# Kernel tuning notes

Hardware: AMD Instinct MI355X
Metric: run time of the kernel (lower is better)

Reference implementation:

```python
import jax, jax.numpy as jnp
import numpy as np

NUM_HEADS = 64
NUM_KV_HEADS = 8
HEAD_DIM = 128
Q_MULT = NUM_HEADS // NUM_KV_HEADS  # 8
CACHE_LEN = 8192
SLIDING_WINDOW = 4096
BATCH = 16
SM_SCALE = 1.0 / float(np.sqrt(HEAD_DIM))


def setup_inputs() -> dict:
    key = jax.random.key(0)
    k1, k2, k3, k4, k5 = jax.random.split(key, 5)
    return {
        "Q": jax.random.normal(k1, (BATCH, 1, NUM_HEADS * HEAD_DIM), dtype=jnp.float32),
        "K": jax.random.normal(k2, (BATCH, 1, NUM_KV_HEADS * HEAD_DIM), dtype=jnp.float32),
        "V": jax.random.normal(k3, (BATCH, 1, NUM_KV_HEADS * HEAD_DIM), dtype=jnp.float32),
        "K_cache": jax.random.normal(k4, (BATCH, CACHE_LEN, NUM_KV_HEADS * HEAD_DIM), dtype=jnp.float32),
        "V_cache": jax.random.normal(k5, (BATCH, CACHE_LEN, NUM_KV_HEADS * HEAD_DIM), dtype=jnp.float32),
        "sinks": jnp.zeros((NUM_HEADS,), dtype=jnp.float32),
    }


def reference(Q, K, V, K_cache, V_cache, sinks):
    B = Q.shape[0]
    total_len = CACHE_LEN + 1
    # reshape to (B, kv_heads, q_mult, d) / (B, len, kv_heads, d)
    q = Q.reshape(B, NUM_KV_HEADS, Q_MULT, HEAD_DIM)
    k_new = K.reshape(B, 1, NUM_KV_HEADS, HEAD_DIM)
    v_new = V.reshape(B, 1, NUM_KV_HEADS, HEAD_DIM)
    k_full = jnp.concatenate([K_cache.reshape(B, CACHE_LEN, NUM_KV_HEADS, HEAD_DIM), k_new], axis=1)
    v_full = jnp.concatenate([V_cache.reshape(B, CACHE_LEN, NUM_KV_HEADS, HEAD_DIM), v_new], axis=1)

    # scores: (B, kv_heads, q_mult, total_len) -- GQA: each kv head serves q_mult query heads
    qk = jnp.einsum("bhmd,bkhd->bhmk", q, k_full) * SM_SCALE

    # sliding-window mask (static shapes: total_len > window here)
    if SLIDING_WINDOW > 0 and total_len > SLIDING_WINDOW:
        pos = jnp.arange(total_len)
        qk = jnp.where(pos[None, None, None, :] < total_len - SLIDING_WINDOW, -jnp.inf, qk)

    # append sink logit per query head, softmax, then drop sink column
    s = sinks.reshape(1, NUM_KV_HEADS, Q_MULT, 1)
    logits = jnp.concatenate([qk, jnp.broadcast_to(s, (B, NUM_KV_HEADS, Q_MULT, 1))], axis=-1)
    w = jax.nn.softmax(logits, axis=-1)[..., :-1]

    attn = jnp.einsum("bhmk,bkhd->bhmd", w, v_full)
    return attn.reshape(B, 1, NUM_HEADS * HEAD_DIM)
```

## Files before the change

kernel.cpp:

```cpp
#include <hip/hip_runtime.h>
#include <math.h>

#define BATCH 16
#define KVH 8
#define QM 8
#define NH 64
#define HD 128
#define CACHE 8192
#define WIN 4096
#define PSTART (CACHE + 1 - WIN)
#define KSTRIDE (KVH * HD)
#define REC_FLOATS (2 * QM + QM * HD)
#define SM_SCALE 0.08838834764831845f

#define BCAST(x, imm) __int_as_float(__builtin_amdgcn_ds_swizzle(__float_as_int(x), (imm)))

#define SCALE_ACC(h, rr) { acc[h].x *= rr; acc[h].y *= rr; acc[h].z *= rr; acc[h].w *= rr; }
#define PV_ACC(h, ww)    { acc[h].x += ww*vc4.x; acc[h].y += ww*vc4.y; acc[h].z += ww*vc4.z; acc[h].w += ww*vc4.w; }

template <int NSPLIT, bool EDGE>
__device__ __forceinline__ void attn_body(
    int c, int b, int t,
    const float* __restrict__ Q, const float* __restrict__ Knew,
    const float* __restrict__ Vnew, const float* __restrict__ Kc,
    const float* __restrict__ Vc, float* __restrict__ ws) {
    constexpr int SPAN = WIN / NSPLIT;
    static_assert(SPAN % 2 == 0, "unroll-2");
    const int g  = t >> 5;
    const int dp = t & 31;
    const int pb = PSTART + c * SPAN;

    float4 q4[8];
    {
        const float* qp = Q + ((size_t)b * NH + (size_t)g * QM) * HD + dp * 4;
        #pragma unroll
        for (int h = 0; h < 8; ++h) {
            float4 v = *reinterpret_cast<const float4*>(qp + h * HD);
            q4[h] = make_float4(v.x * SM_SCALE, v.y * SM_SCALE,
                                v.z * SM_SCALE, v.w * SM_SCALE);
        }
    }

    const float* kb_ = Kc + ((size_t)b * CACHE + pb) * KSTRIDE + t * 4;
    const float* vb_ = Vc + ((size_t)b * CACHE + pb) * KSTRIDE + t * 4;
    const float* kn_ = Knew + (size_t)b * KSTRIDE + t * 4;
    const float* vn_ = Vnew + (size_t)b * KSTRIDE + t * 4;

    auto LK = [&](int j) -> float4 {
        const float* a = kb_ + (size_t)j * KSTRIDE;
        if (EDGE && (pb + j >= CACHE)) a = kn_;
        return *reinterpret_cast<const float4*>(a);
    };
    auto LV = [&](int j) -> float4 {
        const float* a = vb_ + (size_t)j * KSTRIDE;
        if (EDGE && (pb + j >= CACHE)) a = vn_;
        return *reinterpret_cast<const float4*>(a);
    };

    float4 acc[8];
    #pragma unroll
    for (int h = 0; h < 8; ++h) acc[h] = make_float4(0.f, 0.f, 0.f, 0.f);
    float mrun = -INFINITY, lrun = 0.f;

    auto STEP = [&](float4 kc4, float4 vc4) {
        float p0 = q4[0].x*kc4.x + q4[0].y*kc4.y + q4[0].z*kc4.z + q4[0].w*kc4.w;
        float p1 = q4[1].x*kc4.x + q4[1].y*kc4.y + q4[1].z*kc4.z + q4[1].w*kc4.w;
        float p2 = q4[2].x*kc4.x + q4[2].y*kc4.y + q4[2].z*kc4.z + q4[2].w*kc4.w;
        float p3 = q4[3].x*kc4.x + q4[3].y*kc4.y + q4[3].z*kc4.z + q4[3].w*kc4.w;
        float p4 = q4[4].x*kc4.x + q4[4].y*kc4.y + q4[4].z*kc4.z + q4[4].w*kc4.w;
        float p5 = q4[5].x*kc4.x + q4[5].y*kc4.y + q4[5].z*kc4.z + q4[5].w*kc4.w;
        float p6 = q4[6].x*kc4.x + q4[6].y*kc4.y + q4[6].z*kc4.z + q4[6].w*kc4.w;
        float p7 = q4[7].x*kc4.x + q4[7].y*kc4.y + q4[7].z*kc4.z + q4[7].w*kc4.w;
        const bool s1 = dp & 1;
        float a0 = (s1?p1:p0) + __shfl_xor((s1?p0:p1), 1);
        float a1 = (s1?p3:p2) + __shfl_xor((s1?p2:p3), 1);
        float a2 = (s1?p5:p4) + __shfl_xor((s1?p4:p5), 1);
        float a3 = (s1?p7:p6) + __shfl_xor((s1?p6:p7), 1);
        const bool s2 = dp & 2;
        float b0 = (s2?a1:a0) + __shfl_xor((s2?a0:a1), 2);
        float b1 = (s2?a3:a2) + __shfl_xor((s2?a2:a3), 2);
        const bool s4 = dp & 4;
        float s = (s4?b1:b0) + __shfl_xor((s4?b0:b1), 4);
        s += __shfl_xor(s, 8);
        s += __shfl_xor(s, 16);

        if (__any(s > mrun + 8.0f)) {
            float mn = fmaxf(mrun, s);
            float rs = __expf(mrun - mn);
            mrun = mn; lrun *= rs;
            float r0 = BCAST(rs, 0x00); SCALE_ACC(0, r0);
            float r1 = BCAST(rs, 0x20); SCALE_ACC(1, r1);
            float r2 = BCAST(rs, 0x40); SCALE_ACC(2, r2);
            float r3 = BCAST(rs, 0x60); SCALE_ACC(3, r3);
            float r4 = BCAST(rs, 0x80); SCALE_ACC(4, r4);
            float r5 = BCAST(rs, 0xA0); SCALE_ACC(5, r5);
            float r6 = BCAST(rs, 0xC0); SCALE_ACC(6, r6);
            float r7 = BCAST(rs, 0xE0); SCALE_ACC(7, r7);
        }
        float e = __expf(s - mrun);
        lrun += e;
        float w0 = BCAST(e, 0x00); PV_ACC(0, w0);
        float w1 = BCAST(e, 0x20); PV_ACC(1, w1);
        float w2 = BCAST(e, 0x40); PV_ACC(2, w2);
        float w3 = BCAST(e, 0x60); PV_ACC(3, w3);
        float w4 = BCAST(e, 0x80); PV_ACC(4, w4);
        float w5 = BCAST(e, 0xA0); PV_ACC(5, w5);
        float w6 = BCAST(e, 0xC0); PV_ACC(6, w6);
        float w7 = BCAST(e, 0xE0); PV_ACC(7, w7);
    };

    float4 ka = LK(0), va = LV(0), kb4 = LK(1), vb4 = LV(1);
    for (int j = 0; j < SPAN; j += 2) {
        float4 k0 = ka, v0 = va;
        ka = LK(j + 2); va = LV(j + 2);
        STEP(k0, v0);
        float4 k1 = kb4, v1 = vb4;
        kb4 = LK(j + 3); vb4 = LV(j + 3);
        STEP(k1, v1);
    }

    float* rec = ws + ((size_t)(b * KVH + g) * NSPLIT + c) * REC_FLOATS;
    if (dp < 8) { rec[dp] = mrun; rec[QM + dp] = lrun; }
    #pragma unroll
    for (int h = 0; h < 8; ++h)
        *reinterpret_cast<float4*>(rec + 2 * QM + h * HD + dp * 4) = acc[h];
}

template <int NSPLIT>
__global__ __launch_bounds__(256, 4)
void attn_partial(const float* __restrict__ Q, const float* __restrict__ Knew,
                  const float* __restrict__ Vnew, const float* __restrict__ Kc,
                  const float* __restrict__ Vc, float* __restrict__ ws) {
    const int c = blockIdx.x, b = blockIdx.y, t = threadIdx.x;
    if (c == NSPLIT - 1)
        attn_body<NSPLIT, true >(c, b, t, Q, Knew, Vnew, Kc, Vc, ws);
    else
        attn_body<NSPLIT, false>(c, b, t, Q, Knew, Vnew, Kc, Vc, ws);
}

template <int NC>
__global__ __launch_bounds__(256)
void attn_combine(const float* __restrict__ ws, const float* __restrict__ sinks,
                  float* __restrict__ out) {
    const int kvh = blockIdx.x, b = blockIdx.y, t = threadIdx.x;
    const int h = t >> 5, lp = t & 31;
    const float* base = ws + (size_t)(b * KVH + kvh) * NC * REC_FLOATS;

    float M0 = -INFINITY, d0 = 0.f, M1 = -INFINITY, d1 = 0.f;
    float4 o0 = make_float4(0.f, 0.f, 0.f, 0.f);
    float4 o1 = make_float4(0.f, 0.f, 0.f, 0.f);

    #pragma unroll 2
    for (int cc = 0; cc < NC; cc += 2) {
        {
            const float* rec = base + (size_t)cc * REC_FLOATS;
            float mc = rec[h], lc = rec[QM + h];
            float4 a = *reinterpret_cast<const float4*>(rec + 2*QM + h*HD + 4*lp);
            float Mn = fmaxf(M0, mc);
            float fo = __expf(M0 - Mn), fc = __expf(mc - Mn);
            d0 = d0 * fo + fc * lc;
            o0.x = o0.x*fo + fc*a.x; o0.y = o0.y*fo + fc*a.y;
            o0.z = o0.z*fo + fc*a.z; o0.w = o0.w*fo + fc*a.w;
            M0 = Mn;
        }
        {
            const float* rec = base + (size_t)(cc + 1) * REC_FLOATS;
            float mc = rec[h], lc = rec[QM + h];
            float4 a = *reinterpret_cast<const float4*>(rec + 2*QM + h*HD + 4*lp);
            float Mn = fmaxf(M1, mc);
            float fo = __expf(M1 - Mn), fc = __expf(mc - Mn);
            d1 = d1 * fo + fc * lc;
            o1.x = o1.x*fo + fc*a.x; o1.y = o1.y*fo + fc*a.y;
            o1.z = o1.z*fo + fc*a.z; o1.w = o1.w*fo + fc*a.w;
            M1 = Mn;
        }
    }

    const float sk = sinks[kvh * QM + h];
    float M = fmaxf(fmaxf(M0, M1), sk);
    float f0 = __expf(M0 - M), f1 = __expf(M1 - M);
    float d = d0 * f0 + d1 * f1 + __expf(sk - M);
    float inv = 1.f / d;
    float4 r;
    r.x = (o0.x*f0 + o1.x*f1) * inv;
    r.y = (o0.y*f0 + o1.y*f1) * inv;
    r.z = (o0.z*f0 + o1.z*f1) * inv;
    r.w = (o0.w*f0 + o1.w*f1) * inv;
    float* op = out + (size_t)b * NH * HD + (size_t)(kvh * QM + h) * HD + 4 * lp;
    *reinterpret_cast<float4*>(op) = r;
}

template <int NSPLIT>
static void launch_nc(const float* Q, const float* K, const float* V,
                      const float* Kc, const float* Vc, const float* sinks,
                      float* out, float* ws, hipStream_t stream) {
    dim3 g1(NSPLIT, BATCH);
    attn_partial<NSPLIT><<<g1, 256, 0, stream>>>(Q, K, V, Kc, Vc, ws);
    dim3 g2(KVH, BATCH);
    attn_combine<NSPLIT><<<g2, 256, 0, stream>>>(ws, sinks, out);
}

extern "C" void kernel_launch(void* const* d_in, const int* in_sizes, int n_in,
                              void* d_out, int out_size, void* d_ws, size_t ws_size,
                              hipStream_t stream) {
    const float* Q     = (const float*)d_in[0];
    const float* K     = (const float*)d_in[1];
    const float* V     = (const float*)d_in[2];
    const float* Kc    = (const float*)d_in[3];
    const float* Vc    = (const float*)d_in[4];
    const float* sinks = (const float*)d_in[5];
    float* out = (float*)d_out;
    float* ws  = (float*)d_ws;

    auto need = [](int nc) {
        return (size_t)BATCH * KVH * nc * REC_FLOATS * sizeof(float);
    };
    if (ws_size >= need(64))      launch_nc<64>(Q, K, V, Kc, Vc, sinks, out, ws, stream);
    else if (ws_size >= need(32)) launch_nc<32>(Q, K, V, Kc, Vc, sinks, out, ws, stream);
    else                          launch_nc<16>(Q, K, V, Kc, Vc, sinks, out, ws, stream);
}
```

Measured before the change: 122.0 us.

## Parallelize split-K combine with warp-reduced weights and split head-dim grid

The combine kernel now computes the global max and denominator for each query head with warp shuffles, producing normalized per-split weights in shared memory. A serial online-softmax chain over splits is no longer needed. The head dimension is split across a new grid z-dimension of 4, and each block divides the splits among 4 thread groups, summing their partials through LDS. This adds parallelism and removes the dependent exp chain in a small tail kernel, at the cost of extra barriers and redundant weight computation per z-block. The NC=16 fallback is also dropped.

```diff
diff --git a/kernel.cpp b/kernel.cpp
--- a/kernel.cpp
+++ b/kernel.cpp
@@ -142,52 +142,62 @@
 __global__ __launch_bounds__(256)
 void attn_combine(const float* __restrict__ ws, const float* __restrict__ sinks,
                   float* __restrict__ out) {
-    const int kvh = blockIdx.x, b = blockIdx.y, t = threadIdx.x;
-    const int h = t >> 5, lp = t & 31;
+    static_assert(NC == 32 || NC == 64, "NC");
+    const int kvh = blockIdx.x, b = blockIdx.y, ds = blockIdx.z;
+    const int t = threadIdx.x;
     const float* base = ws + (size_t)(b * KVH + kvh) * NC * REC_FLOATS;
 
-    float M0 = -INFINITY, d0 = 0.f, M1 = -INFINITY, d1 = 0.f;
-    float4 o0 = make_float4(0.f, 0.f, 0.f, 0.f);
-    float4 o1 = make_float4(0.f, 0.f, 0.f, 0.f);
-
-    #pragma unroll 2
-    for (int cc = 0; cc < NC; cc += 2) {
-        {
-            const float* rec = base + (size_t)cc * REC_FLOATS;
-            float mc = rec[h], lc = rec[QM + h];
-            float4 a = *reinterpret_cast<const float4*>(rec + 2*QM + h*HD + 4*lp);
-            float Mn = fmaxf(M0, mc);
-            float fo = __expf(M0 - Mn), fc = __expf(mc - Mn);
-            d0 = d0 * fo + fc * lc;
-            o0.x = o0.x*fo + fc*a.x; o0.y = o0.y*fo + fc*a.y;
-            o0.z = o0.z*fo + fc*a.z; o0.w = o0.w*fo + fc*a.w;
-            M0 = Mn;
+    __shared__ float  wlds[QM][65];
+    __shared__ float4 plds[4][64];
+
+    {
+        const int h = t >> 5, lc = t & 31;
+        const float sk = sinks[kvh * QM + h];
+        float m0 = base[(size_t)lc * REC_FLOATS + h];
+        float l0 = base[(size_t)lc * REC_FLOATS + QM + h];
+        float m1 = -INFINITY, l1 = 0.f;
+        if constexpr (NC == 64) {
+            m1 = base[(size_t)(lc + 32) * REC_FLOATS + h];
+            l1 = base[(size_t)(lc + 32) * REC_FLOATS + QM + h];
         }
-        {
-            const float* rec = base + (size_t)(cc + 1) * REC_FLOATS;
-            float mc = rec[h], lc = rec[QM + h];
-            float4 a = *reinterpret_cast<const float4*>(rec + 2*QM + h*HD + 4*lp);
-            float Mn = fmaxf(M1, mc);
-            float fo = __expf(M1 - Mn), fc = __expf(mc - Mn);
-            d1 = d1 * fo + fc * lc;
-            o1.x = o1.x*fo + fc*a.x; o1.y = o1.y*fo + fc*a.y;
-            o1.z = o1.z*fo + fc*a.z; o1.w = o1.w*fo + fc*a.w;
-            M1 = Mn;
-        }
-    }
-
-    const float sk = sinks[kvh * QM + h];
-    float M = fmaxf(fmaxf(M0, M1), sk);
-    float f0 = __expf(M0 - M), f1 = __expf(M1 - M);
-    float d = d0 * f0 + d1 * f1 + __expf(sk - M);
-    float inv = 1.f / d;
-    float4 r;
-    r.x = (o0.x*f0 + o1.x*f1) * inv;
-    r.y = (o0.y*f0 + o1.y*f1) * inv;
-    r.z = (o0.z*f0 + o1.z*f1) * inv;
-    r.w = (o0.w*f0 + o1.w*f1) * inv;
-    float* op = out + (size_t)b * NH * HD + (size_t)(kvh * QM + h) * HD + 4 * lp;
-    *reinterpret_cast<float4*>(op) = r;
+        float M = fmaxf(fmaxf(m0, m1), sk);
+        #pragma unroll
+        for (int off = 16; off; off >>= 1) M = fmaxf(M, __shfl_xor(M, off));
+        float f0 = __expf(m0 - M);
+        float f1 = (NC == 64) ? __expf(m1 - M) : 0.f;
+        float dsum = f0 * l0 + f1 * l1;
+        #pragma unroll
+        for (int off = 16; off; off >>= 1) dsum += __shfl_xor(dsum, off);
+        float inv = 1.f / (dsum + __expf(sk - M));
+        wlds[h][lc] = f0 * inv;
+        if constexpr (NC == 64) wlds[h][lc + 32] = f1 * inv;
+    }
+    __syncthreads();
+
+    const int qd  = (t & 7) + 8 * ds;
+    const int h   = (t >> 3) & 7;
+    const int par = t >> 6;
+    float4 o = make_float4(0.f, 0.f, 0.f, 0.f);
+    #pragma unroll 4
+    for (int c = par; c < NC; c += 4) {
+        float w = wlds[h][c];
+        const float* ap = base + (size_t)c * REC_FLOATS + 2 * QM + h * HD + 4 * qd;
+        float4 a = *reinterpret_cast<const float4*>(ap);
+        o.x += w * a.x; o.y += w * a.y; o.z += w * a.z; o.w += w * a.w;
+    }
+    plds[par][t & 63] = o;
+    __syncthreads();
+    if (t < 64) {
+        float4 r0 = plds[0][t], r1 = plds[1][t], r2 = plds[2][t], r3 = plds[3][t];
+        float4 r;
+        r.x = (r0.x + r1.x) + (r2.x + r3.x);
+        r.y = (r0.y + r1.y) + (r2.y + r3.y);
+        r.z = (r0.z + r1.z) + (r2.z + r3.z);
+        r.w = (r0.w + r1.w) + (r2.w + r3.w);
+        const int hh = (t >> 3) & 7, qq = (t & 7) + 8 * ds;
+        float* op = out + (size_t)b * NH * HD + (size_t)(kvh * QM + hh) * HD + 4 * qq;
+        *reinterpret_cast<float4*>(op) = r;
+    }
 }
 
 template <int NSPLIT>
@@ -196,7 +206,7 @@
                       float* out, float* ws, hipStream_t stream) {
     dim3 g1(NSPLIT, BATCH);
     attn_partial<NSPLIT><<<g1, 256, 0, stream>>>(Q, K, V, Kc, Vc, ws);
-    dim3 g2(KVH, BATCH);
+    dim3 g2(KVH, BATCH, 4);
     attn_combine<NSPLIT><<<g2, 256, 0, stream>>>(ws, sinks, out);
 }
 
@@ -215,7 +225,6 @@
     auto need = [](int nc) {
         return (size_t)BATCH * KVH * nc * REC_FLOATS * sizeof(float);
     };
-    if (ws_size >= need(64))      launch_nc<64>(Q, K, V, Kc, Vc, sinks, out, ws, stream);
-    else if (ws_size >= need(32)) launch_nc<32>(Q, K, V, Kc, Vc, sinks, out, ws, stream);
-    else                          launch_nc<16>(Q, K, V, Kc, Vc, sinks, out, ws, stream);
-}
+    if (ws_size >= need(64)) launch_nc<64>(Q, K, V, Kc, Vc, sinks, out, ws, stream);
+    else                     launch_nc<32>(Q, K, V, Kc, Vc, sinks, out, ws, stream);
+}
```

Measured after the change: 121.4 us. No clear change (-0.5%).
